# Optimization experiments

Measured on AMD Instinct MI355X. Metric: run time of the kernel, lower is better.

The kernel has to match this reference:

```python
import jax, jax.numpy as jnp
import numpy as np

N, D, H, K = 4096, 256, 4, 16

def setup_inputs() -> dict:
    key = jax.random.key(0)
    ks = jax.random.split(key, 6)
    return {
        "query":     jax.random.normal(ks[0], (N, D), dtype=jnp.float32),
        "key_value": jax.random.normal(ks[1], (N, D), dtype=jnp.float32),
        "W_q": jax.random.normal(ks[2], (H, D, K), dtype=jnp.float32) * 0.05,
        "W_k": jax.random.normal(ks[3], (H, D, K), dtype=jnp.float32) * 0.05,
        "W_v": jax.random.normal(ks[4], (H, D, K), dtype=jnp.float32) * 0.05,
        "W_o": jax.random.normal(ks[5], (H * K, D), dtype=jnp.float32) * 0.05,
    }

def reference(query, key_value, W_q, W_k, W_v, W_o):
    # Per-head projections, batched over heads: [H, N, K]
    Q = jnp.einsum('nd,hdk->hnk', query, W_q)
    Kh = jnp.einsum('nd,hdk->hnk', key_value, W_k)
    V = jnp.einsum('nd,hdk->hnk', key_value, W_v)
    scale = jnp.sqrt(jnp.asarray(K, dtype=Q.dtype))
    scores = jnp.einsum('hnk,hmk->hnm', Q, Kh) / scale  # [H, N, N]
    attn = jax.nn.softmax(scores, axis=-1)
    heads = jnp.einsum('hnm,hmk->hnk', attn, V)         # [H, N, K]
    # concat heads along last dim (head-major order) -> [N, H*K]
    concat = jnp.transpose(heads, (1, 0, 2)).reshape(query.shape[0], -1)
    return concat @ W_o  # [N, D]
```

## Files before the change

### kernel.cpp

```cpp
#include <hip/hip_runtime.h>

#define NN 4096
#define DD 256
#define HH 4
#define KK 16
#define SPLIT 4

typedef short bf16x4 __attribute__((ext_vector_type(4)));
typedef float f32x4 __attribute__((ext_vector_type(4)));

__device__ __forceinline__ unsigned short f2bf(float f) {
  unsigned int u = __float_as_uint(f);
  u += 0x7fffu + ((u >> 16) & 1u);
  return (unsigned short)(u >> 16);
}

__device__ __forceinline__ float fexp2(float x) {
#if __has_builtin(__builtin_amdgcn_exp2f)
  return __builtin_amdgcn_exp2f(x);
#else
  return exp2f(x);
#endif
}

__device__ __forceinline__ f32x4 mfma16_bf16(bf16x4 a, bf16x4 b, f32x4 c) {
#if __has_builtin(__builtin_amdgcn_mfma_f32_16x16x16bf16_1k)
  return __builtin_amdgcn_mfma_f32_16x16x16bf16_1k(a, b, c, 0, 0, 0);
#else
  f32x4 d;
  asm volatile("v_mfma_f32_16x16x16_bf16 %0, %1, %2, %3\n\ts_nop 7\n\ts_nop 7"
               : "=&v"(d) : "v"(a), "v"(b), "v"(c));
  return d;
#endif
}

__global__ __launch_bounds__(64) void wfrag_kernel(
    const float* __restrict__ Wq, const float* __restrict__ Wk,
    const float* __restrict__ Wv, unsigned short* __restrict__ wf) {
  const int b = blockIdx.x;
  const int mat = b >> 6, h = (b >> 4) & 3, kstep = b & 15;
  const int l = threadIdx.x;
  const int lx = l & 15, g = l >> 4;
  const float* W = (mat == 0) ? Wq : (mat == 1 ? Wk : Wv);
  const float scale = (mat == 0) ? 0.25f * 1.4426950408889634f : 1.0f;
  unsigned short* dst = wf + ((size_t)b * 64 + l) * 4;
  #pragma unroll
  for (int j = 0; j < 4; j++) {
    int d = kstep * 16 + g * 4 + j;
    dst[j] = f2bf(W[(size_t)h * DD * KK + (size_t)d * KK + lx] * scale);
  }
}

__global__ __launch_bounds__(256) void proj_gemm_kernel(
    const float* __restrict__ query, const float* __restrict__ kvin,
    const unsigned short* __restrict__ wf,
    unsigned short* __restrict__ Qb, unsigned short* __restrict__ Kb,
    unsigned short* __restrict__ Vb) {
  const int tid = threadIdx.x;
  const int w = tid >> 6, l = tid & 63;
  const int lx = l & 15, g = l >> 4;
  const int id = blockIdx.x * 4 + w;
  const int qt = id / 12, ns = id % 12;
  const int mat = ns >> 2, h = ns & 3;
  const float* src = (mat == 0) ? query : kvin;
  const unsigned short* wfb = wf + (size_t)((mat * 4 + h) * 16) * 64 * 4;
  const float* arow = src + (size_t)(qt * 16 + lx) * DD + g * 4;

  f32x4 acc = {0.f, 0.f, 0.f, 0.f};
  #pragma unroll
  for (int ks = 0; ks < 16; ks++) {
    float4 a0 = *(const float4*)(arow + ks * 16);
    bf16x4 af;
    af[0] = (short)f2bf(a0.x); af[1] = (short)f2bf(a0.y);
    af[2] = (short)f2bf(a0.z); af[3] = (short)f2bf(a0.w);
    bf16x4 bfr = *(const bf16x4*)(wfb + ((size_t)ks * 64 + l) * 4);
    acc = mfma16_bf16(af, bfr, acc);
  }
  unsigned short* dstp = (mat == 0) ? Qb : (mat == 1 ? Kb : Vb);
  #pragma unroll
  for (int r = 0; r < 4; r++) {
    int n = qt * 16 + g * 4 + r;
    dstp[((size_t)h * NN + n) * KK + lx] = f2bf(acc[r]);
  }
}

__global__ __launch_bounds__(256) void attn_kernel(
    const unsigned short* __restrict__ Qb, const unsigned short* __restrict__ Kb,
    const unsigned short* __restrict__ Vb, float* __restrict__ pbuf) {
  __shared__ unsigned short vt[16 * 1024];
  const int tid = threadIdx.x;
  const int w = tid >> 6, l = tid & 63;
  const int lx = l & 15, g = l >> 4;
  const int h = blockIdx.y, sp = blockIdx.z;
  const int kb0 = sp * (NN / SPLIT);
  const int q0 = blockIdx.x * 128 + w * 32;

  for (int i = tid; i < 4096; i += 256) {
    int key = i >> 2, v0 = (i & 3) * 4;
    uint2 u = *(const uint2*)(Vb + ((size_t)h * NN + kb0 + key) * KK + v0);
    #pragma unroll
    for (int m = 0; m < 4; m++) {
      int v = v0 + m;
      unsigned short val = (unsigned short)((m < 2 ? u.x : u.y) >> ((m & 1) * 16));
      int byteoff = (v << 11) + ((((key >> 2) ^ v) & 255) << 3) + ((key & 3) << 1);
      *(unsigned short*)((char*)vt + byteoff) = val;
    }
  }
  __syncthreads();

  bf16x4 qfa = *(const bf16x4*)(Qb + ((size_t)h * NN + q0 + lx) * KK + g * 4);
  bf16x4 qfb = *(const bf16x4*)(Qb + ((size_t)h * NN + q0 + 16 + lx) * KK + g * 4);

  const unsigned short* kptr = Kb + ((size_t)h * NN + kb0 + lx) * KK + g * 4;
  f32x4 c2a = {0.f, 0.f, 0.f, 0.f}, c2b = {0.f, 0.f, 0.f, 0.f};
  const f32x4 zero4 = {0.f, 0.f, 0.f, 0.f};
  float ssa = 0.f, ssb = 0.f;

  #pragma unroll 2
  for (int tile = 0; tile < 64; tile++) {
    bf16x4 kf = *(const bf16x4*)kptr;
    kptr += 256;
    int gran = ((tile << 2) + g) ^ lx;
    bf16x4 vf = *(const bf16x4*)((char*)vt + (lx << 11) + (gran << 3));

    f32x4 c1a = mfma16_bf16(kf, qfa, zero4);
    f32x4 c1b = mfma16_bf16(kf, qfb, zero4);
    bf16x4 pa, pb;
    #pragma unroll
    for (int r = 0; r < 4; r++) {
      float ea = fexp2(c1a[r]);
      float eb = fexp2(c1b[r]);
      ssa += ea; ssb += eb;
      pa[r] = (short)f2bf(ea);
      pb[r] = (short)f2bf(eb);
    }
    c2a = mfma16_bf16(vf, pa, c2a);
    c2b = mfma16_bf16(vf, pb, c2b);
  }

  ssa += __shfl_xor(ssa, 16); ssa += __shfl_xor(ssa, 32);
  ssb += __shfl_xor(ssb, 16); ssb += __shfl_xor(ssb, 32);

  size_t ba = ((size_t)(h * NN + q0 + lx) * SPLIT + sp) * 17;
  size_t bb = ((size_t)(h * NN + q0 + 16 + lx) * SPLIT + sp) * 17;
  #pragma unroll
  for (int r = 0; r < 4; r++) {
    pbuf[ba + g * 4 + r] = c2a[r];
    pbuf[bb + g * 4 + r] = c2b[r];
  }
  if (g == 0) { pbuf[ba + 16] = ssa; pbuf[bb + 16] = ssb; }
}

__global__ __launch_bounds__(256) void reduce_out_kernel(
    const float* __restrict__ pbuf, const float* __restrict__ Wo,
    float* __restrict__ out) {
  __shared__ float cc[8][64];
  const int tid = threadIdx.x;
  const int n0  = blockIdx.x * 8;

  for (int it = tid; it < 512; it += 256) {
    int r = it >> 6;
    int j = it & 63;
    int h = j >> 4;
    int kk2 = j & 15;
    size_t hn = (size_t)h * NN + n0 + r;
    float num = 0.f, den = 0.f;
    #pragma unroll
    for (int s2 = 0; s2 < SPLIT; s2++) {
      const float* p = pbuf + (hn * SPLIT + s2) * 17;
      num += p[kk2];
      den += p[16];
    }
    cc[r][j] = num / den;
  }
  __syncthreads();

  float acc[8];
  #pragma unroll
  for (int r = 0; r < 8; r++) acc[r] = 0.f;
  for (int j = 0; j < 64; j++) {
    float wv = Wo[(size_t)j * DD + tid];
    #pragma unroll
    for (int r = 0; r < 8; r++) acc[r] = fmaf(cc[r][j], wv, acc[r]);
  }
  #pragma unroll
  for (int r = 0; r < 8; r++)
    out[(size_t)(n0 + r) * DD + tid] = acc[r];
}

extern "C" void kernel_launch(void* const* d_in, const int* in_sizes, int n_in,
                              void* d_out, int out_size, void* d_ws, size_t ws_size,
                              hipStream_t stream) {
  const float* query = (const float*)d_in[0];
  const float* kv    = (const float*)d_in[1];
  const float* Wq    = (const float*)d_in[2];
  const float* Wk    = (const float*)d_in[3];
  const float* Wv    = (const float*)d_in[4];
  const float* Wo    = (const float*)d_in[5];
  float* out = (float*)d_out;

  unsigned short* Qb = (unsigned short*)d_ws;
  unsigned short* Kb = Qb + (size_t)HH * NN * KK;
  unsigned short* Vb = Kb + (size_t)HH * NN * KK;
  unsigned short* wf = Vb + (size_t)HH * NN * KK;
  float* pbuf = (float*)((char*)d_ws +
                         2u * (3u * HH * NN * KK + 192u * 64u * 4u));

  hipLaunchKernelGGL(wfrag_kernel, dim3(192), dim3(64), 0, stream, Wq, Wk, Wv, wf);
  hipLaunchKernelGGL(proj_gemm_kernel, dim3(768), dim3(256), 0, stream,
                     query, kv, wf, Qb, Kb, Vb);
  hipLaunchKernelGGL(attn_kernel, dim3(NN / 128, HH, SPLIT), dim3(256), 0, stream,
                     Qb, Kb, Vb, pbuf);
  hipLaunchKernelGGL(reduce_out_kernel, dim3(NN / 8), dim3(256), 0, stream,
                     pbuf, Wo, out);
}
```

Measured before the change: 110.0 us.

## Store V transposed from projection, drop LDS staging, double key split

The projection kernel now writes V transposed ([H, K, N]) so the attention kernel reads V fragments directly from global memory. This removes the shared-memory transpose staging and the block barrier. The key-split factor rises from 4 to 8, doubling the attention grid while halving the tiles per block, and the loop unroll goes from 2 to 4. Risks: the transposed V stores are strided and uncoalesced, and the partial buffer and the reduce kernel's traffic both double.

```diff
diff --git a/kernel.cpp b/kernel.cpp
--- a/kernel.cpp
+++ b/kernel.cpp
@@ -1,18 +1,18 @@
 #include <hip/hip_runtime.h>
+#include <hip/hip_bf16.h>
 
 #define NN 4096
 #define DD 256
 #define HH 4
 #define KK 16
-#define SPLIT 4
+#define SPLIT 8
 
 typedef short bf16x4 __attribute__((ext_vector_type(4)));
 typedef float f32x4 __attribute__((ext_vector_type(4)));
 
-__device__ __forceinline__ unsigned short f2bf(float f) {
-  unsigned int u = __float_as_uint(f);
-  u += 0x7fffu + ((u >> 16) & 1u);
-  return (unsigned short)(u >> 16);
+__device__ __forceinline__ unsigned short bf16c(float f) {
+  __hip_bfloat16 h = __float2bfloat16(f);
+  return *reinterpret_cast<unsigned short*>(&h);
 }
 
 __device__ __forceinline__ float fexp2(float x) {
@@ -47,7 +47,7 @@
   #pragma unroll
   for (int j = 0; j < 4; j++) {
     int d = kstep * 16 + g * 4 + j;
-    dst[j] = f2bf(W[(size_t)h * DD * KK + (size_t)d * KK + lx] * scale);
+    dst[j] = bf16c(W[(size_t)h * DD * KK + (size_t)d * KK + lx] * scale);
   }
 }
 
@@ -55,7 +55,7 @@
     const float* __restrict__ query, const float* __restrict__ kvin,
     const unsigned short* __restrict__ wf,
     unsigned short* __restrict__ Qb, unsigned short* __restrict__ Kb,
-    unsigned short* __restrict__ Vb) {
+    unsigned short* __restrict__ Vt) {
   const int tid = threadIdx.x;
   const int w = tid >> 6, l = tid & 63;
   const int lx = l & 15, g = l >> 4;
@@ -71,23 +71,30 @@
   for (int ks = 0; ks < 16; ks++) {
     float4 a0 = *(const float4*)(arow + ks * 16);
     bf16x4 af;
-    af[0] = (short)f2bf(a0.x); af[1] = (short)f2bf(a0.y);
-    af[2] = (short)f2bf(a0.z); af[3] = (short)f2bf(a0.w);
+    af[0] = (short)bf16c(a0.x); af[1] = (short)bf16c(a0.y);
+    af[2] = (short)bf16c(a0.z); af[3] = (short)bf16c(a0.w);
     bf16x4 bfr = *(const bf16x4*)(wfb + ((size_t)ks * 64 + l) * 4);
     acc = mfma16_bf16(af, bfr, acc);
   }
-  unsigned short* dstp = (mat == 0) ? Qb : (mat == 1 ? Kb : Vb);
-  #pragma unroll
-  for (int r = 0; r < 4; r++) {
-    int n = qt * 16 + g * 4 + r;
-    dstp[((size_t)h * NN + n) * KK + lx] = f2bf(acc[r]);
+  if (mat < 2) {
+    unsigned short* dstp = (mat == 0) ? Qb : Kb;
+    #pragma unroll
+    for (int r = 0; r < 4; r++) {
+      int n = qt * 16 + g * 4 + r;
+      dstp[((size_t)h * NN + n) * KK + lx] = bf16c(acc[r]);
+    }
+  } else {
+    #pragma unroll
+    for (int r = 0; r < 4; r++) {
+      int n = qt * 16 + g * 4 + r;
+      Vt[((size_t)h * KK + lx) * NN + n] = bf16c(acc[r]);
+    }
   }
 }
 
 __global__ __launch_bounds__(256) void attn_kernel(
     const unsigned short* __restrict__ Qb, const unsigned short* __restrict__ Kb,
-    const unsigned short* __restrict__ Vb, float* __restrict__ pbuf) {
-  __shared__ unsigned short vt[16 * 1024];
+    const unsigned short* __restrict__ Vt, float* __restrict__ pbuf) {
   const int tid = threadIdx.x;
   const int w = tid >> 6, l = tid & 63;
   const int lx = l & 15, g = l >> 4;
@@ -95,33 +102,21 @@
   const int kb0 = sp * (NN / SPLIT);
   const int q0 = blockIdx.x * 128 + w * 32;
 
-  for (int i = tid; i < 4096; i += 256) {
-    int key = i >> 2, v0 = (i & 3) * 4;
-    uint2 u = *(const uint2*)(Vb + ((size_t)h * NN + kb0 + key) * KK + v0);
-    #pragma unroll
-    for (int m = 0; m < 4; m++) {
-      int v = v0 + m;
-      unsigned short val = (unsigned short)((m < 2 ? u.x : u.y) >> ((m & 1) * 16));
-      int byteoff = (v << 11) + ((((key >> 2) ^ v) & 255) << 3) + ((key & 3) << 1);
-      *(unsigned short*)((char*)vt + byteoff) = val;
-    }
-  }
-  __syncthreads();
-
   bf16x4 qfa = *(const bf16x4*)(Qb + ((size_t)h * NN + q0 + lx) * KK + g * 4);
   bf16x4 qfb = *(const bf16x4*)(Qb + ((size_t)h * NN + q0 + 16 + lx) * KK + g * 4);
 
   const unsigned short* kptr = Kb + ((size_t)h * NN + kb0 + lx) * KK + g * 4;
+  const unsigned short* vptr = Vt + ((size_t)h * KK + lx) * NN + kb0 + g * 4;
   f32x4 c2a = {0.f, 0.f, 0.f, 0.f}, c2b = {0.f, 0.f, 0.f, 0.f};
   const f32x4 zero4 = {0.f, 0.f, 0.f, 0.f};
   float ssa = 0.f, ssb = 0.f;
 
-  #pragma unroll 2
-  for (int tile = 0; tile < 64; tile++) {
+  #pragma unroll 4
+  for (int tile = 0; tile < NN / SPLIT / 16; tile++) {
     bf16x4 kf = *(const bf16x4*)kptr;
-    kptr += 256;
-    int gran = ((tile << 2) + g) ^ lx;
-    bf16x4 vf = *(const bf16x4*)((char*)vt + (lx << 11) + (gran << 3));
+    kptr += 16 * KK;
+    bf16x4 vf = *(const bf16x4*)vptr;
+    vptr += 16;
 
     f32x4 c1a = mfma16_bf16(kf, qfa, zero4);
     f32x4 c1b = mfma16_bf16(kf, qfb, zero4);
@@ -131,8 +126,8 @@
       float ea = fexp2(c1a[r]);
       float eb = fexp2(c1b[r]);
       ssa += ea; ssb += eb;
-      pa[r] = (short)f2bf(ea);
-      pb[r] = (short)f2bf(eb);
+      pa[r] = (short)bf16c(ea);
+      pb[r] = (short)bf16c(eb);
     }
     c2a = mfma16_bf16(vf, pa, c2a);
     c2b = mfma16_bf16(vf, pb, c2b);
@@ -201,16 +196,16 @@
 
   unsigned short* Qb = (unsigned short*)d_ws;
   unsigned short* Kb = Qb + (size_t)HH * NN * KK;
-  unsigned short* Vb = Kb + (size_t)HH * NN * KK;
-  unsigned short* wf = Vb + (size_t)HH * NN * KK;
+  unsigned short* Vt = Kb + (size_t)HH * NN * KK;
+  unsigned short* wf = Vt + (size_t)HH * NN * KK;
   float* pbuf = (float*)((char*)d_ws +
                          2u * (3u * HH * NN * KK + 192u * 64u * 4u));
 
   hipLaunchKernelGGL(wfrag_kernel, dim3(192), dim3(64), 0, stream, Wq, Wk, Wv, wf);
   hipLaunchKernelGGL(proj_gemm_kernel, dim3(768), dim3(256), 0, stream,
-                     query, kv, wf, Qb, Kb, Vb);
+                     query, kv, wf, Qb, Kb, Vt);
   hipLaunchKernelGGL(attn_kernel, dim3(NN / 128, HH, SPLIT), dim3(256), 0, stream,
-                     Qb, Kb, Vb, pbuf);
+                     Qb, Kb, Vt, pbuf);
   hipLaunchKernelGGL(reduce_out_kernel, dim3(NN / 8), dim3(256), 0, stream,
                      pbuf, Wo, out);
 }
```

Measured after the change: 109.0 us. No clear change (-1.0%).
